# Kernel tuning notes

Hardware: AMD Instinct MI355X
Metric: run time of the kernel (lower is better)

## Reference

```python
import jax, jax.numpy as jnp
import numpy as np

EMB = 1024
HEADS = 16
HEAD_DIM = EMB // HEADS
B, T = 2, 2048
LN_EPS = 1e-5  # torch nn.LayerNorm default


def _layernorm(x, g, b):
    # LayerNorm over last dim (head_dim), elementwise affine
    mu = jnp.mean(x, axis=-1, keepdims=True)
    var = jnp.mean(jnp.square(x - mu), axis=-1, keepdims=True)
    return (x - mu) * jax.lax.rsqrt(var + LN_EPS) * g + b


def setup_inputs() -> dict:
    key = jax.random.key(0)
    ks = jax.random.split(key, 6)
    sc = 1.0 / np.sqrt(EMB)  # keep linear outputs O(1)
    return {
        "x": jax.random.normal(ks[0], (B, T, EMB), dtype=jnp.float32),
        "Wk": jax.random.normal(ks[1], (EMB, EMB), dtype=jnp.float32) * sc,
        "Wq": jax.random.normal(ks[2], (EMB, EMB), dtype=jnp.float32) * sc,
        "Wv": jax.random.normal(ks[3], (EMB, EMB), dtype=jnp.float32) * sc,
        "Wu": jax.random.normal(ks[4], (EMB, EMB), dtype=jnp.float32) * sc,
        "bu": jnp.zeros((EMB,), dtype=jnp.float32),
        "kln_g": jnp.ones((HEAD_DIM,), dtype=jnp.float32),
        "kln_b": jnp.zeros((HEAD_DIM,), dtype=jnp.float32),
        "qln_g": jnp.ones((HEAD_DIM,), dtype=jnp.float32),
        "qln_b": jnp.zeros((HEAD_DIM,), dtype=jnp.float32),
    }


def reference(x, Wk, Wq, Wv, Wu, bu, kln_g, kln_b, qln_g, qln_b):
    b, t, e = x.shape
    h, s = HEADS, HEAD_DIM
    # torch Linear (no bias): y = x @ W.T
    keys = (x @ Wk.T).reshape(b, t, h, s)
    queries = (x @ Wq.T).reshape(b, t, h, s)
    values = (x @ Wv.T).reshape(b, t, h, s)
    # per-head LayerNorm (kqnorm=True)
    keys = _layernorm(keys, kln_g, kln_b)
    queries = _layernorm(queries, qln_g, qln_b)
    # NOTE: module scales by emb**(-1/4) on each side (net 1/sqrt(emb), not head dim)
    inv4 = e ** (-0.25)
    queries = queries * inv4
    keys = keys * inv4
    # scores: [b, h, t, t]
    dot = jnp.einsum('bqhs,bkhs->bhqk', queries, keys)
    # causal mask: positions k > q set to -inf (mask_diagonal=False -> diag kept)
    causal = jnp.tril(jnp.ones((t, t), dtype=bool))
    dot = jnp.where(causal, dot, -jnp.inf)
    attn = jax.nn.softmax(dot, axis=-1)
    out = jnp.einsum('bhqk,bkhs->bqhs', attn, values).reshape(b, t, h * s)
    return out @ Wu.T + bu
```

## Files before the change

### kernel.cpp

```cpp
#include <hip/hip_runtime.h>
#include <math.h>

#define EMB 1024
#define NHEADS 16
#define HDIM 64
#define BATCH 2
#define SEQ 2048
#define MROWS (BATCH*SEQ)
#define LN_EPS 1e-5f
#define GK 1024
#define GN 1024

typedef __attribute__((ext_vector_type(8))) short bf16x8;
typedef __attribute__((ext_vector_type(4))) short s16x4;
typedef __attribute__((ext_vector_type(4))) float f32x4;
typedef __attribute__((ext_vector_type(16))) float f32x16;
typedef __attribute__((ext_vector_type(4))) int int4v;

__device__ __forceinline__ short f2bf(float f) {
    union { float f; unsigned u; } v; v.f = f;
    unsigned r = v.u + 0x7FFFu + ((v.u >> 16) & 1u);
    return (short)(r >> 16);
}
__device__ __forceinline__ float bf2f(short s) {
    union { unsigned u; float f; } v; v.u = ((unsigned)(unsigned short)s) << 16;
    return v.f;
}
__device__ __forceinline__ unsigned cvtpk(float a, float b) {
    unsigned r;
    asm("v_cvt_pk_bf16_f32 %0, %1, %2" : "=v"(r) : "v"(a), "v"(b));
    return r;
}
__device__ __forceinline__ float fexp2(float x) {
    return __builtin_amdgcn_exp2f(x);
}

__device__ __forceinline__ void gload16(const short* g, short* l) {
    __builtin_amdgcn_global_load_lds(
        (const __attribute__((address_space(1))) unsigned*)g,
        (__attribute__((address_space(3))) unsigned*)l, 16, 0, 0);
}

#define MFMA32(a, b, c) __builtin_amdgcn_mfma_f32_32x32x16_bf16(a, b, c, 0, 0, 0)

#define SRC_G(r, c)  ((((c) - ((r) >> 1)) & 3) * 8)
#define RD_G(r, l4)  ((((l4) + ((r) >> 1)) & 3) * 8)

__global__ __launch_bounds__(256)
void cvt_all(const float* __restrict__ X, short* __restrict__ XH,
             const float* __restrict__ W0, const float* __restrict__ W1,
             const float* __restrict__ W2, const float* __restrict__ W3,
             short* __restrict__ WH)
{
    const int zy = blockIdx.y;
    if (zy == 0) {
        const size_t i = (size_t)blockIdx.x * 1024 + threadIdx.x * 4;
        const float4 v = *(const float4*)&X[i];
        s16x4 h;
        h[0] = f2bf(v.x); h[1] = f2bf(v.y);
        h[2] = f2bf(v.z); h[3] = f2bf(v.w);
        *(s16x4*)&XH[i] = h;
    } else {
        const int z = zy - 1;
        if (blockIdx.x >= 1024) return;
        const float* W = (z == 0) ? W0 : (z == 1) ? W1 : (z == 2) ? W2 : W3;
        const size_t i = (size_t)blockIdx.x * 1024 + threadIdx.x * 4;
        const float4 v = *(const float4*)&W[i];
        s16x4 h;
        h[0] = f2bf(v.x); h[1] = f2bf(v.y);
        h[2] = f2bf(v.z); h[3] = f2bf(v.w);
        *(s16x4*)&WH[((size_t)z << 20) + i] = h;
    }
}

__global__ __launch_bounds__(256, 3)
void gemm_kqv(const short* __restrict__ Xh, const short* __restrict__ W4h,
              const float* __restrict__ kg, const float* __restrict__ kb,
              const float* __restrict__ qg, const float* __restrict__ qb,
              float scaleK, float scaleQ,
              short* __restrict__ KhP, short* __restrict__ QhP,
              short* __restrict__ VTh)
{
    __shared__ short AhS[3][128][32], BhS[3][128][32];

    const int t   = threadIdx.x;
    const int ln  = t & 63, wv = t >> 6;
    const int l15 = ln & 15, l4 = ln >> 4;
    const int m0  = blockIdx.y * 128;
    const int n0  = blockIdx.x * 128;
    const int z   = blockIdx.z;
    const int wr  = (wv >> 1) * 64, wc = (wv & 1) * 64;

    const short* Bh = W4h + ((size_t)z << 20);

    const short* gplane = (wv < 2) ? Xh : Bh;
    const int    grow0  = (wv < 2) ? m0 : n0;
    short* lbase = (wv < 2) ? &AhS[0][0][0] : &BhS[0][0][0];
    const int s0 = (wv & 1) ? 4 : 0;

    f32x4 acc[4][4];
    #pragma unroll
    for (int i = 0; i < 4; ++i)
        #pragma unroll
        for (int j = 0; j < 4; ++j) acc[i][j] = (f32x4){0.f, 0.f, 0.f, 0.f};

    #pragma unroll
    for (int s = 0; s < 4; ++s) {
        const int chunk = (s0 + s) * 64 + ln;
        const int r = chunk >> 2, c = chunk & 3;
        gload16(gplane + (size_t)(grow0 + r) * GK + SRC_G(r, c),
                lbase + (s0 + s) * 512);
    }
    #pragma unroll
    for (int s = 0; s < 4; ++s) {
        const int chunk = (s0 + s) * 64 + ln;
        const int r = chunk >> 2, c = chunk & 3;
        gload16(gplane + (size_t)(grow0 + r) * GK + 32 + SRC_G(r, c),
                lbase + 4096 + (s0 + s) * 512);
    }
    asm volatile("s_waitcnt vmcnt(4)" ::: "memory");
    __builtin_amdgcn_s_barrier();

    int cur = 0;
    for (int i = 0; i < 32; ++i) {
        const int cur2 = (cur == 0) ? 2 : cur - 1;
        if (i + 2 < 32) {
            short* lp = lbase + cur2 * 4096;
            const int kof = (i + 2) * 32;
            #pragma unroll
            for (int s = 0; s < 4; ++s) {
                const int chunk = (s0 + s) * 64 + ln;
                const int r = chunk >> 2, c = chunk & 3;
                gload16(gplane + (size_t)(grow0 + r) * GK + kof + SRC_G(r, c),
                        lp + (s0 + s) * 512);
            }
        }

        bf16x8 ah[4], bh[4];
        #pragma unroll
        for (int f = 0; f < 4; ++f) {
            const int ra = wr + f * 16 + l15;
            const int rb = wc + f * 16 + l15;
            ah[f] = *(const bf16x8*)&AhS[cur][ra][RD_G(ra, l4)];
            bh[f] = *(const bf16x8*)&BhS[cur][rb][RD_G(rb, l4)];
        }
        #pragma unroll
        for (int i2 = 0; i2 < 4; ++i2)
            #pragma unroll
            for (int j = 0; j < 4; ++j)
                acc[i2][j] = __builtin_amdgcn_mfma_f32_16x16x32_bf16(ah[i2], bh[j], acc[i2][j], 0, 0, 0);

        if (i + 2 < 32) {
            asm volatile("s_waitcnt vmcnt(4)" ::: "memory");
        } else if (i + 1 < 32) {
            asm volatile("s_waitcnt vmcnt(0)" ::: "memory");
        }
        __builtin_amdgcn_s_barrier();
        cur = (cur == 2) ? 0 : cur + 1;
    }

    if (z < 2) {
        const float* gamma = (z == 0) ? kg : qg;
        const float* beta  = (z == 0) ? kb : qb;
        short* OutH = (z == 0) ? KhP : QhP;
        const float scl = (z == 0) ? scaleK : scaleQ;
        const int n_head = (n0 + wc) >> 6;
        float g4[4], b4[4];
        #pragma unroll
        for (int f = 0; f < 4; ++f) {
            g4[f] = gamma[f * 16 + l15];
            b4[f] = beta [f * 16 + l15];
        }
        #pragma unroll
        for (int i = 0; i < 4; ++i)
            #pragma unroll
            for (int j = 0; j < 4; ++j) {
                const float v0 = acc[i][0][j], v1 = acc[i][1][j];
                const float v2 = acc[i][2][j], v3 = acc[i][3][j];
                float s1 = v0 + v1 + v2 + v3;
                float s2 = v0*v0 + v1*v1 + v2*v2 + v3*v3;
                s1 += __shfl_xor(s1, 1); s2 += __shfl_xor(s2, 1);
                s1 += __shfl_xor(s1, 2); s2 += __shfl_xor(s2, 2);
                s1 += __shfl_xor(s1, 4); s2 += __shfl_xor(s2, 4);
                s1 += __shfl_xor(s1, 8); s2 += __shfl_xor(s2, 8);
                const float mu  = s1 * (1.f / 64.f);
                const float var = s2 * (1.f / 64.f) - mu * mu;
                const float rs  = rsqrtf(var + LN_EPS);
                const int m = m0 + wr + i * 16 + l4 * 4 + j;
                const size_t orow =
                    ((size_t)((m >> 11) * NHEADS + n_head) * SEQ + (m & (SEQ - 1))) * HDIM;
                #pragma unroll
                for (int f = 0; f < 4; ++f) {
                    const float y = ((acc[i][f][j] - mu) * rs * g4[f] + b4[f]) * scl;
                    OutH[orow + f * 16 + l15] = f2bf(y);
                }
            }
    } else {
        #pragma unroll
        for (int i = 0; i < 4; ++i)
            #pragma unroll
            for (int f = 0; f < 4; ++f) {
                s16x4 h4;
                #pragma unroll
                for (int j = 0; j < 4; ++j) h4[j] = f2bf(acc[i][f][j]);
                const int n  = n0 + wc + f * 16 + l15;
                const int hh = n >> 6, dd = n & 63;
                const int mb = m0 + wr + i * 16 + l4 * 4;
                const size_t oa =
                    (((size_t)((mb >> 11) * NHEADS + hh)) * HDIM + dd) * SEQ + (mb & (SEQ - 1));
                *(s16x4*)&VTh[oa] = h4;
            }
    }
}

__global__ __launch_bounds__(256, 2)
void gemm_out(const short* __restrict__ Ah, const short* __restrict__ Bh,
              const float* __restrict__ bias, float* __restrict__ OutF)
{
    __shared__ short AhS[2][64][32], BhS[2][128][32];

    const int t   = threadIdx.x;
    const int ln  = t & 63, wv = t >> 6;
    const int l15 = ln & 15, l4 = ln >> 4;
    const int m0  = blockIdx.y * 64;
    const int n0  = blockIdx.x * 128;
    const int wr  = (wv >> 1) * 32, wc = (wv & 1) * 64;

    const short* gplane = (wv == 0) ? Ah : Bh;
    const int    grow0  = (wv == 0) ? m0 : n0;
    const int    s0     = (wv == 2) ? 4 : 0;
    const int    nseg   = (wv < 3) ? 4 : 0;
    const int    bstep  = (wv == 0) ? 2048 : 4096;
    short* lbase = (wv == 0) ? &AhS[0][0][0] : &BhS[0][0][0];

    f32x4 acc[2][4];
    #pragma unroll
    for (int i = 0; i < 2; ++i)
        #pragma unroll
        for (int j = 0; j < 4; ++j) acc[i][j] = (f32x4){0.f, 0.f, 0.f, 0.f};

    for (int s = 0; s < nseg; ++s) {
        const int chunk = (s0 + s) * 64 + ln;
        const int r = chunk >> 2, c = chunk & 3;
        gload16(gplane + (size_t)(grow0 + r) * GK + SRC_G(r, c),
                lbase + (s0 + s) * 512);
    }
    __syncthreads();

    int cur = 0;
    for (int k0 = 0; k0 < GK; k0 += 32) {
        if (k0 + 32 < GK) {
            short* lp = lbase + (cur ^ 1) * bstep;
            for (int s = 0; s < nseg; ++s) {
                const int chunk = (s0 + s) * 64 + ln;
                const int r = chunk >> 2, c = chunk & 3;
                gload16(gplane + (size_t)(grow0 + r) * GK + k0 + 32 + SRC_G(r, c),
                        lp + (s0 + s) * 512);
            }
        }

        bf16x8 ah[2], bh[4];
        #pragma unroll
        for (int f = 0; f < 2; ++f) {
            const int ra = wr + f * 16 + l15;
            ah[f] = *(const bf16x8*)&AhS[cur][ra][RD_G(ra, l4)];
        }
        #pragma unroll
        for (int f = 0; f < 4; ++f) {
            const int rb = wc + f * 16 + l15;
            bh[f] = *(const bf16x8*)&BhS[cur][rb][RD_G(rb, l4)];
        }
        #pragma unroll
        for (int i = 0; i < 2; ++i)
            #pragma unroll
            for (int j = 0; j < 4; ++j)
                acc[i][j] = __builtin_amdgcn_mfma_f32_16x16x32_bf16(ah[i], bh[j], acc[i][j], 0, 0, 0);

        __syncthreads();
        cur ^= 1;
    }

    float b4[4];
    #pragma unroll
    for (int f = 0; f < 4; ++f) b4[f] = bias[n0 + wc + f * 16 + l15];
    #pragma unroll
    for (int i = 0; i < 2; ++i)
        #pragma unroll
        for (int j = 0; j < 4; ++j) {
            const int m = m0 + wr + i * 16 + l4 * 4 + j;
            const size_t row = (size_t)m * GN + n0 + wc;
            #pragma unroll
            for (int f = 0; f < 4; ++f)
                OutF[row + f * 16 + l15] = acc[i][f][j] + b4[f];
        }
}

__global__ __launch_bounds__(256, 2)
void attn_mfma(const short* __restrict__ Qh, const short* __restrict__ Kh,
               const short* __restrict__ Vh, short* __restrict__ Oh)
{
    __shared__ short KhS[2][64][64];
    __shared__ short VhS[2][64][64];

    const int t    = threadIdx.x;
    const int lane = t & 63, wv = t >> 6;
    const int l31  = lane & 31, hb = lane >> 5;

    const int lin = (int)blockIdx.y * 16 + (int)blockIdx.x;
    const int xcd = lin & 7;
    const int m   = lin >> 3;
    const int bh  = xcd * 4 + (m >> 4);
    const int qtr = m & 15;
    const int qt  = ((m >> 5) & 1) ? qtr : 15 - qtr;

    const int bb   = bh >> 4, hh = bh & 15;
    const int q0   = qt * 128;
    const int wq0  = wv * 32;

    const size_t kpan = (size_t)bh * SEQ * HDIM;
    const size_t vpan = (size_t)bh * HDIM * SEQ;

    const int sr0  = t >> 3, sr1 = 32 + (t >> 3);
    const int scg  = t & 7;
    const int soff = scg * 8;
    const int lc0  = (scg ^ (sr0 & 7)) * 8;

    bf16x8 qfh[4];
    {
        const size_t qrow = kpan + (size_t)(q0 + wq0 + l31) * HDIM;
        #pragma unroll
        for (int ds = 0; ds < 4; ++ds)
            qfh[ds] = *(const bf16x8*)&Qh[qrow + ds * 16 + hb * 8];
    }

    f32x16 oacc0 = (f32x16)(0.0f), oacc1 = (f32x16)(0.0f);
    float m_run = -1e30f, l_run = 0.f;

    const int NR = qt + 1;

    int4v pK[2][2], pV[2][2];
    #pragma unroll
    for (int h = 0; h < 2; ++h) {
        const int kb0 = h * 64;
        pK[h][0] = *(const int4v*)&Kh[kpan + (size_t)(kb0 + sr0) * HDIM + soff];
        pK[h][1] = *(const int4v*)&Kh[kpan + (size_t)(kb0 + sr1) * HDIM + soff];
        pV[h][0] = *(const int4v*)&Vh[vpan + (size_t)sr0 * SEQ + kb0 + soff];
        pV[h][1] = *(const int4v*)&Vh[vpan + (size_t)sr1 * SEQ + kb0 + soff];
    }

    for (int rr = 0; rr < NR; ++rr) {
        const int k0 = rr * 128;

        __syncthreads();

        #pragma unroll
        for (int h = 0; h < 2; ++h) {
            *(int4v*)&KhS[h][sr0][lc0] = pK[h][0];
            *(int4v*)&KhS[h][sr1][lc0] = pK[h][1];
            *(int4v*)&VhS[h][sr0][lc0] = pV[h][0];
            *(int4v*)&VhS[h][sr1][lc0] = pV[h][1];
        }

        if (rr + 1 < NR) {
            const int kn = k0 + 128;
            #pragma unroll
            for (int h = 0; h < 2; ++h) {
                const int kb0 = kn + h * 64;
                pK[h][0] = *(const int4v*)&Kh[kpan + (size_t)(kb0 + sr0) * HDIM + soff];
                pK[h][1] = *(const int4v*)&Kh[kpan + (size_t)(kb0 + sr1) * HDIM + soff];
                pV[h][0] = *(const int4v*)&Vh[vpan + (size_t)sr0 * SEQ + kb0 + soff];
                pV[h][1] = *(const int4v*)&Vh[vpan + (size_t)sr1 * SEQ + kb0 + soff];
            }
        }
        __syncthreads();

        #pragma unroll
        for (int half = 0; half < 2; ++half) {
            const int kk0 = k0 + half * 64;
            if (kk0 > q0 + wq0 + 31) continue;

            f32x16 s0 = (f32x16)(0.0f), s1 = (f32x16)(0.0f);
            #pragma unroll
            for (int ds = 0; ds < 4; ++ds) {
                const int g = ((ds * 2 + hb) ^ (l31 & 7)) * 8;
                const bf16x8 kh0 = *(const bf16x8*)&KhS[half][l31][g];
                const bf16x8 kh1 = *(const bf16x8*)&KhS[half][32 + l31][g];
                s0 = MFMA32(kh0, qfh[ds], s0);
                s1 = MFMA32(kh1, qfh[ds], s1);
            }

            if (kk0 + 63 > q0 + wq0) {
                const int qg = q0 + wq0 + l31;
                #pragma unroll
                for (int reg = 0; reg < 16; ++reg) {
                    const int kk = kk0 + (reg & 3) + 8 * (reg >> 2) + 4 * hb;
                    if (kk > qg)      s0[reg] = -1e30f;
                    if (kk + 32 > qg) s1[reg] = -1e30f;
                }
            }

            {
                float mx = -1e30f;
                #pragma unroll
                for (int reg = 0; reg < 16; ++reg)
                    mx = fmaxf(mx, fmaxf(s0[reg], s1[reg]));
                mx = fmaxf(mx, __shfl_xor(mx, 32));
                if (__any(mx > m_run)) {
                    const float mnew = fmaxf(m_run, mx);
                    const float scf  = fexp2(m_run - mnew);
                    m_run = mnew;
                    l_run *= scf;
                    #pragma unroll
                    for (int reg = 0; reg < 16; ++reg) {
                        oacc0[reg] *= scf;
                        oacc1[reg] *= scf;
                    }
                }
                float ls = 0.f;
                #pragma unroll
                for (int reg = 0; reg < 16; ++reg) {
                    const float p0 = fexp2(s0[reg] - m_run);
                    const float p1 = fexp2(s1[reg] - m_run);
                    s0[reg] = p0; s1[reg] = p1;
                    ls += p0 + p1;
                }
                ls += __shfl_xor(ls, 32);
                l_run += ls;
            }

            #pragma unroll
            for (int ks = 0; ks < 4; ++ks) {
                const int sb = (ks & 1) * 8;
                unsigned hA0, hA1, hB0, hB1;
                if (ks >= 2) {
                    hA0 = cvtpk(s1[sb + 0], s1[sb + 1]);
                    hA1 = cvtpk(s1[sb + 2], s1[sb + 3]);
                    hB0 = cvtpk(s1[sb + 4], s1[sb + 5]);
                    hB1 = cvtpk(s1[sb + 6], s1[sb + 7]);
                } else {
                    hA0 = cvtpk(s0[sb + 0], s0[sb + 1]);
                    hA1 = cvtpk(s0[sb + 2], s0[sb + 3]);
                    hB0 = cvtpk(s0[sb + 4], s0[sb + 5]);
                    hB1 = cvtpk(s0[sb + 6], s0[sb + 7]);
                }
                const unsigned hr0 = (unsigned)__shfl_xor((int)(hb ? hA0 : hB0), 32);
                const unsigned hr1 = (unsigned)__shfl_xor((int)(hb ? hA1 : hB1), 32);
                const int4v wih = (int4v){(int)(hb ? hr0 : hA0), (int)(hb ? hr1 : hA1),
                                          (int)(hb ? hB0 : hr0), (int)(hb ? hB1 : hr1)};
                const bf16x8 pfh = __builtin_bit_cast(bf16x8, wih);

                const int gv = ((ks * 2 + hb) ^ (l31 & 7)) * 8;
                const bf16x8 vh0 = *(const bf16x8*)&VhS[half][l31][gv];
                const bf16x8 vh1 = *(const bf16x8*)&VhS[half][32 + l31][gv];
                oacc0 = MFMA32(vh0, pfh, oacc0);
                oacc1 = MFMA32(vh1, pfh, oacc1);
            }
        }
    }

    const float inv = 1.f / l_run;
    const int q = q0 + wq0 + l31;
    const size_t row = ((size_t)(bb * SEQ + q)) * EMB + hh * HDIM;
    #pragma unroll
    for (int db = 0; db < 2; ++db)
        #pragma unroll
        for (int b = 0; b < 4; ++b) {
            const float v0 = (db ? oacc1[4 * b + 0] : oacc0[4 * b + 0]) * inv;
            const float v1 = (db ? oacc1[4 * b + 1] : oacc0[4 * b + 1]) * inv;
            const float v2 = (db ? oacc1[4 * b + 2] : oacc0[4 * b + 2]) * inv;
            const float v3 = (db ? oacc1[4 * b + 3] : oacc0[4 * b + 3]) * inv;
            uint2 w2;
            w2.x = cvtpk(v0, v1);
            w2.y = cvtpk(v2, v3);
            const int d0 = db * 32 + 8 * b + 4 * hb;
            *(uint2*)&Oh[row + d0] = w2;
        }
}

extern "C" void kernel_launch(void* const* d_in, const int* in_sizes, int n_in,
                              void* d_out, int out_size, void* d_ws, size_t ws_size,
                              hipStream_t stream)
{
    const float* x  = (const float*)d_in[0];
    const float* Wk = (const float*)d_in[1];
    const float* Wq = (const float*)d_in[2];
    const float* Wv = (const float*)d_in[3];
    const float* Wu = (const float*)d_in[4];
    const float* bu = (const float*)d_in[5];
    const float* kg = (const float*)d_in[6];
    const float* kb = (const float*)d_in[7];
    const float* qg = (const float*)d_in[8];
    const float* qb = (const float*)d_in[9];
    float* out = (float*)d_out;

    char* w = (char*)d_ws;
    short* XhP = (short*)(w);
    short* KhP = (short*)(w + (8u  << 20));
    short* QhP = (short*)(w + (16u << 20));
    short* W4h = (short*)(w + (24u << 20));
    short* VTh = (short*)d_out;

    const float inv4 = 0.17677669529663687f;
    const float l2e  = 1.4426950408889634f;

    cvt_all<<<dim3(4096, 5), 256, 0, stream>>>(x, XhP, Wk, Wq, Wv, Wu, W4h);

    gemm_kqv<<<dim3(GN / 128, MROWS / 128, 3), 256, 0, stream>>>(
        XhP, W4h, kg, kb, qg, qb, inv4, inv4 * l2e,
        KhP, QhP, VTh);

    attn_mfma<<<dim3(SEQ / 128, BATCH * NHEADS), 256, 0, stream>>>(
        QhP, KhP, VTh, XhP);

    gemm_out<<<dim3(GN / 128, MROWS / 64), 256, 0, stream>>>(
        XhP, W4h + (3u << 20), bu, out);
}
```

Before: 113.4 us.

## Split attention key tiles across two wave groups with LDS merge

Doubles the attention block to 512 threads. Each of the two wave groups handles one 32-key half of every 64-key subtile for the same query stripe, keeping its own online-softmax state. At the end the partial outputs and max/sum statistics are merged through shared memory. The aim is more waves in flight and less serial per-wave work per query stripe, paid for by an extra sync, LDS traffic for the merge, and bf16 rounding of one group's partial accumulators.

```diff
diff --git a/kernel.cpp b/kernel.cpp
--- a/kernel.cpp
+++ b/kernel.cpp
@@ -295,7 +295,7 @@
         }
 }
 
-__global__ __launch_bounds__(256, 2)
+__global__ __launch_bounds__(512, 4)
 void attn_mfma(const short* __restrict__ Qh, const short* __restrict__ Kh,
                const short* __restrict__ Vh, short* __restrict__ Oh)
 {
@@ -305,6 +305,7 @@
     const int t    = threadIdx.x;
     const int lane = t & 63, wv = t >> 6;
     const int l31  = lane & 31, hb = lane >> 5;
+    const int stripe = wv & 3, kh2 = wv >> 2;
 
     const int lin = (int)blockIdx.y * 16 + (int)blockIdx.x;
     const int xcd = lin & 7;
@@ -315,13 +316,14 @@
 
     const int bb   = bh >> 4, hh = bh & 15;
     const int q0   = qt * 128;
-    const int wq0  = wv * 32;
+    const int wq0  = stripe * 32;
 
     const size_t kpan = (size_t)bh * SEQ * HDIM;
     const size_t vpan = (size_t)bh * HDIM * SEQ;
 
-    const int sr0  = t >> 3, sr1 = 32 + (t >> 3);
-    const int scg  = t & 7;
+    const int u    = t & 255, u8 = t >> 8;
+    const int sr0  = u >> 3, sr1 = 32 + (u >> 3);
+    const int scg  = u & 7;
     const int soff = scg * 8;
     const int lc0  = (scg ^ (sr0 & 7)) * 8;
 
@@ -338,14 +340,13 @@
 
     const int NR = qt + 1;
 
-    int4v pK[2][2], pV[2][2];
-    #pragma unroll
-    for (int h = 0; h < 2; ++h) {
-        const int kb0 = h * 64;
-        pK[h][0] = *(const int4v*)&Kh[kpan + (size_t)(kb0 + sr0) * HDIM + soff];
-        pK[h][1] = *(const int4v*)&Kh[kpan + (size_t)(kb0 + sr1) * HDIM + soff];
-        pV[h][0] = *(const int4v*)&Vh[vpan + (size_t)sr0 * SEQ + kb0 + soff];
-        pV[h][1] = *(const int4v*)&Vh[vpan + (size_t)sr1 * SEQ + kb0 + soff];
+    int4v pK0, pK1, pV0, pV1;
+    {
+        const int kb0 = u8 * 64;
+        pK0 = *(const int4v*)&Kh[kpan + (size_t)(kb0 + sr0) * HDIM + soff];
+        pK1 = *(const int4v*)&Kh[kpan + (size_t)(kb0 + sr1) * HDIM + soff];
+        pV0 = *(const int4v*)&Vh[vpan + (size_t)sr0 * SEQ + kb0 + soff];
+        pV1 = *(const int4v*)&Vh[vpan + (size_t)sr1 * SEQ + kb0 + soff];
     }
 
     for (int rr = 0; rr < NR; ++rr) {
@@ -353,57 +354,46 @@
 
         __syncthreads();
 
-        #pragma unroll
-        for (int h = 0; h < 2; ++h) {
-            *(int4v*)&KhS[h][sr0][lc0] = pK[h][0];
-            *(int4v*)&KhS[h][sr1][lc0] = pK[h][1];
-            *(int4v*)&VhS[h][sr0][lc0] = pV[h][0];
-            *(int4v*)&VhS[h][sr1][lc0] = pV[h][1];
-        }
+        *(int4v*)&KhS[u8][sr0][lc0] = pK0;
+        *(int4v*)&KhS[u8][sr1][lc0] = pK1;
+        *(int4v*)&VhS[u8][sr0][lc0] = pV0;
+        *(int4v*)&VhS[u8][sr1][lc0] = pV1;
 
         if (rr + 1 < NR) {
-            const int kn = k0 + 128;
-            #pragma unroll
-            for (int h = 0; h < 2; ++h) {
-                const int kb0 = kn + h * 64;
-                pK[h][0] = *(const int4v*)&Kh[kpan + (size_t)(kb0 + sr0) * HDIM + soff];
-                pK[h][1] = *(const int4v*)&Kh[kpan + (size_t)(kb0 + sr1) * HDIM + soff];
-                pV[h][0] = *(const int4v*)&Vh[vpan + (size_t)sr0 * SEQ + kb0 + soff];
-                pV[h][1] = *(const int4v*)&Vh[vpan + (size_t)sr1 * SEQ + kb0 + soff];
-            }
+            const int kb0 = k0 + 128 + u8 * 64;
+            pK0 = *(const int4v*)&Kh[kpan + (size_t)(kb0 + sr0) * HDIM + soff];
+            pK1 = *(const int4v*)&Kh[kpan + (size_t)(kb0 + sr1) * HDIM + soff];
+            pV0 = *(const int4v*)&Vh[vpan + (size_t)sr0 * SEQ + kb0 + soff];
+            pV1 = *(const int4v*)&Vh[vpan + (size_t)sr1 * SEQ + kb0 + soff];
         }
         __syncthreads();
 
         #pragma unroll
         for (int half = 0; half < 2; ++half) {
-            const int kk0 = k0 + half * 64;
-            if (kk0 > q0 + wq0 + 31) continue;
-
-            f32x16 s0 = (f32x16)(0.0f), s1 = (f32x16)(0.0f);
+            const int kw0 = k0 + half * 64 + kh2 * 32;
+            if (kw0 > q0 + wq0 + 31) continue;
+
+            f32x16 s = (f32x16)(0.0f);
             #pragma unroll
             for (int ds = 0; ds < 4; ++ds) {
                 const int g = ((ds * 2 + hb) ^ (l31 & 7)) * 8;
-                const bf16x8 kh0 = *(const bf16x8*)&KhS[half][l31][g];
-                const bf16x8 kh1 = *(const bf16x8*)&KhS[half][32 + l31][g];
-                s0 = MFMA32(kh0, qfh[ds], s0);
-                s1 = MFMA32(kh1, qfh[ds], s1);
-            }
-
-            if (kk0 + 63 > q0 + wq0) {
+                const bf16x8 kf = *(const bf16x8*)&KhS[half][kh2 * 32 + l31][g];
+                s = MFMA32(kf, qfh[ds], s);
+            }
+
+            if (kw0 + 31 > q0 + wq0) {
                 const int qg = q0 + wq0 + l31;
                 #pragma unroll
                 for (int reg = 0; reg < 16; ++reg) {
-                    const int kk = kk0 + (reg & 3) + 8 * (reg >> 2) + 4 * hb;
-                    if (kk > qg)      s0[reg] = -1e30f;
-                    if (kk + 32 > qg) s1[reg] = -1e30f;
+                    const int kk = kw0 + (reg & 3) + 8 * (reg >> 2) + 4 * hb;
+                    if (kk > qg) s[reg] = -1e30f;
                 }
             }
 
             {
                 float mx = -1e30f;
                 #pragma unroll
-                for (int reg = 0; reg < 16; ++reg)
-                    mx = fmaxf(mx, fmaxf(s0[reg], s1[reg]));
+                for (int reg = 0; reg < 16; ++reg) mx = fmaxf(mx, s[reg]);
                 mx = fmaxf(mx, __shfl_xor(mx, 32));
                 if (__any(mx > m_run)) {
                     const float mnew = fmaxf(m_run, mx);
@@ -419,30 +409,22 @@
                 float ls = 0.f;
                 #pragma unroll
                 for (int reg = 0; reg < 16; ++reg) {
-                    const float p0 = fexp2(s0[reg] - m_run);
-                    const float p1 = fexp2(s1[reg] - m_run);
-                    s0[reg] = p0; s1[reg] = p1;
-                    ls += p0 + p1;
+                    const float p = fexp2(s[reg] - m_run);
+                    s[reg] = p;
+                    ls += p;
                 }
                 ls += __shfl_xor(ls, 32);
                 l_run += ls;
             }
 
             #pragma unroll
-            for (int ks = 0; ks < 4; ++ks) {
-                const int sb = (ks & 1) * 8;
-                unsigned hA0, hA1, hB0, hB1;
-                if (ks >= 2) {
-                    hA0 = cvtpk(s1[sb + 0], s1[sb + 1]);
-                    hA1 = cvtpk(s1[sb + 2], s1[sb + 3]);
-                    hB0 = cvtpk(s1[sb + 4], s1[sb + 5]);
-                    hB1 = cvtpk(s1[sb + 6], s1[sb + 7]);
-                } else {
-                    hA0 = cvtpk(s0[sb + 0], s0[sb + 1]);
-                    hA1 = cvtpk(s0[sb + 2], s0[sb + 3]);
-                    hB0 = cvtpk(s0[sb + 4], s0[sb + 5]);
-                    hB1 = cvtpk(s0[sb + 6], s0[sb + 7]);
-                }
+            for (int ks2 = 0; ks2 < 2; ++ks2) {
+                const int ks = kh2 * 2 + ks2;
+                const int sb = ks2 * 8;
+                const unsigned hA0 = cvtpk(s[sb + 0], s[sb + 1]);
+                const unsigned hA1 = cvtpk(s[sb + 2], s[sb + 3]);
+                const unsigned hB0 = cvtpk(s[sb + 4], s[sb + 5]);
+                const unsigned hB1 = cvtpk(s[sb + 6], s[sb + 7]);
                 const unsigned hr0 = (unsigned)__shfl_xor((int)(hb ? hA0 : hB0), 32);
                 const unsigned hr1 = (unsigned)__shfl_xor((int)(hb ? hA1 : hB1), 32);
                 const int4v wih = (int4v){(int)(hb ? hr0 : hA0), (int)(hb ? hr1 : hA1),
@@ -458,23 +440,56 @@
         }
     }
 
-    const float inv = 1.f / l_run;
-    const int q = q0 + wq0 + l31;
-    const size_t row = ((size_t)(bb * SEQ + q)) * EMB + hh * HDIM;
-    #pragma unroll
-    for (int db = 0; db < 2; ++db)
-        #pragma unroll
-        for (int b = 0; b < 4; ++b) {
-            const float v0 = (db ? oacc1[4 * b + 0] : oacc0[4 * b + 0]) * inv;
-            const float v1 = (db ? oacc1[4 * b + 1] : oacc0[4 * b + 1]) * inv;
-            const float v2 = (db ? oacc1[4 * b + 2] : oacc0[4 * b + 2]) * inv;
-            const float v3 = (db ? oacc1[4 * b + 3] : oacc0[4 * b + 3]) * inv;
-            uint2 w2;
-            w2.x = cvtpk(v0, v1);
-            w2.y = cvtpk(v2, v3);
-            const int d0 = db * 32 + 8 * b + 4 * hb;
-            *(uint2*)&Oh[row + d0] = w2;
-        }
+    __syncthreads();
+    unsigned* oscr = (unsigned*)&KhS[0][0][0];
+    float*    mls  = (float*)&VhS[0][0][0];
+
+    if (kh2 == 1) {
+        const int base = (stripe * 64 + lane) * 16;
+        #pragma unroll
+        for (int i = 0; i < 8; ++i)
+            oscr[base + i]     = cvtpk(oacc0[2 * i], oacc0[2 * i + 1]);
+        #pragma unroll
+        for (int i = 0; i < 8; ++i)
+            oscr[base + 8 + i] = cvtpk(oacc1[2 * i], oacc1[2 * i + 1]);
+        mls[(stripe * 64 + lane) * 2]     = m_run;
+        mls[(stripe * 64 + lane) * 2 + 1] = l_run;
+    }
+    __syncthreads();
+
+    if (kh2 == 0) {
+        const float mB = mls[(stripe * 64 + lane) * 2];
+        const float lB = mls[(stripe * 64 + lane) * 2 + 1];
+        const float mm = fmaxf(m_run, mB);
+        const float fa = fexp2(m_run - mm);
+        const float fb = fexp2(mB - mm);
+        const float inv = 1.f / (l_run * fa + lB * fb);
+        const int base = (stripe * 64 + lane) * 16;
+
+        const int q = q0 + wq0 + l31;
+        const size_t row = ((size_t)(bb * SEQ + q)) * EMB + hh * HDIM;
+        #pragma unroll
+        for (int db = 0; db < 2; ++db)
+            #pragma unroll
+            for (int b = 0; b < 4; ++b) {
+                const int pi = db * 8 + 2 * b;
+                const unsigned uB0 = oscr[base + pi];
+                const unsigned uB1 = oscr[base + pi + 1];
+                const float a0 = (db ? oacc1[4 * b + 0] : oacc0[4 * b + 0]);
+                const float a1 = (db ? oacc1[4 * b + 1] : oacc0[4 * b + 1]);
+                const float a2 = (db ? oacc1[4 * b + 2] : oacc0[4 * b + 2]);
+                const float a3 = (db ? oacc1[4 * b + 3] : oacc0[4 * b + 3]);
+                const float v0 = (a0 * fa + bf2f((short)(uB0 & 0xffff))  * fb) * inv;
+                const float v1 = (a1 * fa + bf2f((short)(uB0 >> 16))    * fb) * inv;
+                const float v2 = (a2 * fa + bf2f((short)(uB1 & 0xffff)) * fb) * inv;
+                const float v3 = (a3 * fa + bf2f((short)(uB1 >> 16))    * fb) * inv;
+                uint2 w2;
+                w2.x = cvtpk(v0, v1);
+                w2.y = cvtpk(v2, v3);
+                const int d0 = db * 32 + 8 * b + 4 * hb;
+                *(uint2*)&Oh[row + d0] = w2;
+            }
+    }
 }
 
 extern "C" void kernel_launch(void* const* d_in, const int* in_sizes, int n_in,
@@ -509,7 +524,7 @@
         XhP, W4h, kg, kb, qg, qb, inv4, inv4 * l2e,
         KhP, QhP, VTh);
 
-    attn_mfma<<<dim3(SEQ / 128, BATCH * NHEADS), 256, 0, stream>>>(
+    attn_mfma<<<dim3(SEQ / 128, BATCH * NHEADS), 512, 0, stream>>>(
         QhP, KhP, VTh, XhP);
 
     gemm_out<<<dim3(GN / 128, MROWS / 64), 256, 0, stream>>>(
```

Result: faster. 109.2 us (-3.7%).
